# Kernel optimization log

Hardware: AMD Instinct MI355X
Metric: run time of the kernel (lower is better)

The kernel has to match this reference:

```python
import math
import jax, jax.numpy as jnp
import numpy as np

B, S, H = 4, 2048, 1024      # batch, seq_len, hidden_size
E, K, I = 8, 2, 1024         # n_routed_experts, top_k, expert intermediate
NSH = 2                      # n_shared_experts -> shared intermediate = NSH*I
CF, RSF = 1.25, 1.0          # capacity_factor, routed_scaling_factor


def setup_inputs() -> dict:
    key = jax.random.key(0)
    ks = jax.random.split(key, 8)
    w = lambda k, sh: jax.random.normal(k, sh, dtype=jnp.float32) * 0.02
    return {
        "hidden_states": jax.random.normal(ks[0], (B, S, H), dtype=jnp.float32),
        "gate_w":  w(ks[1], (E, H)),          # router weight (torch Linear layout)
        "we_gate": w(ks[2], (E, I, H)),       # per-expert gate_proj
        "we_up":   w(ks[3], (E, I, H)),       # per-expert up_proj
        "we_down": w(ks[4], (E, H, I)),       # per-expert down_proj
        "ws_gate": w(ks[5], (NSH * I, H)),    # shared expert gate_proj
        "ws_up":   w(ks[6], (NSH * I, H)),
        "ws_down": w(ks[7], (H, NSH * I)),
    }


def reference(hidden_states, gate_w, we_gate, we_up, we_down, ws_gate, ws_up, ws_down):
    orig_shape = hidden_states.shape
    x = hidden_states.reshape(-1, H)                       # [N, H]
    N = x.shape[0]

    # ---- gate (fp32 softmax + top-k, normalized, scaled) ----
    logits = x.astype(jnp.float32) @ gate_w.astype(jnp.float32).T   # [N, E]
    scores = jax.nn.softmax(logits, axis=-1)
    topk_w, topk_idx = jax.lax.top_k(scores, K)                      # [N, K]
    topk_w = topk_w / (topk_w.sum(-1, keepdims=True) + 1e-20) * RSF  # norm_topk_prob

    # ---- capacity masking: position of each (token,k) slot within its expert ----
    capacity = math.ceil(CF * N * K / E)
    flat = topk_idx.reshape(-1)                                      # [N*K]
    one_hot = jax.nn.one_hot(flat, E, dtype=jnp.int32)               # [N*K, E]
    pos = jnp.cumsum(one_hot, axis=0) - 1                            # running count per expert
    pos_tok = jnp.take_along_axis(pos, flat[:, None], axis=1)[:, 0]  # [N*K]
    keep = (pos_tok < capacity).reshape(N, K)
    topk_w = topk_w * keep.astype(topk_w.dtype)

    # ---- combine weights per (token, expert); dropped slots contribute 0 ----
    comb = jnp.zeros((N, E), jnp.float32).at[jnp.arange(N)[:, None], topk_idx].add(topk_w)

    # ---- routed experts: dense SwiGLU per expert, weighted combine ----
    g = jnp.einsum('nh,eih->nei', x, we_gate)                        # [N, E, I]
    u = jnp.einsum('nh,eih->nei', x, we_up)
    eo = jnp.einsum('nei,ehi->neh', jax.nn.silu(g) * u, we_down)     # [N, E, H]
    y = jnp.einsum('neh,ne->nh', eo, comb)                           # [N, H]

    # ---- shared experts ----
    sh = (jax.nn.silu(x @ ws_gate.T) * (x @ ws_up.T)) @ ws_down.T    # [N, H]

    return (y + sh).reshape(orig_shape)
```

## Files before the change

### kernel.cpp

```cpp
#include <hip/hip_runtime.h>

typedef unsigned short u16;

#define NTOK 8192
#define HD   1024
#define NEXP 8
#define CAP  2560

typedef __bf16 bf16x8 __attribute__((ext_vector_type(8)));
typedef float  f32x4  __attribute__((ext_vector_type(4)));

__device__ __forceinline__ u16 f2bf(float f){
  union { float f; unsigned u; } v; v.f = f;
  return (u16)((v.u + 0x7fffu + ((v.u >> 16) & 1u)) >> 16);
}
__device__ __forceinline__ float bf2f(u16 h){
  union { unsigned u; float f; } v; v.u = ((unsigned)h) << 16; return v.f;
}

__device__ __forceinline__ void async16(const void* g, void* l){
  __builtin_amdgcn_global_load_lds((__attribute__((address_space(1))) void*)(g),
                                   (__attribute__((address_space(3))) void*)(l), 16, 0, 0);
}

__global__ __launch_bounds__(256)
void prep_kernel(const float* __restrict__ x, const float* __restrict__ gate_w,
                 const float* __restrict__ we_gate, const float* __restrict__ we_up,
                 const float* __restrict__ we_down, const float* __restrict__ ws_gate,
                 const float* __restrict__ ws_up, const float* __restrict__ ws_down,
                 u16* __restrict__ x_bf, u16* __restrict__ wg_bf, u16* __restrict__ wu_bf,
                 u16* __restrict__ wd_bf, u16* __restrict__ wsg_bf, u16* __restrict__ wsu_bf,
                 u16* __restrict__ wsd_bf,
                 int* __restrict__ topk_idx, float* __restrict__ topk_w){
  __shared__ float gw[NEXP * HD];
  int bid = blockIdx.x;
  int t = threadIdx.x;
  if (bid < 2048){
    for (int i = t; i < NEXP * HD; i += 256) gw[i] = gate_w[i];
    __syncthreads();
    int wave = t >> 6, l = t & 63;
    int tok = bid * 4 + wave;
    const float* xr = x + (size_t)tok * HD;
    double acc[NEXP];
#pragma unroll
    for (int e = 0; e < NEXP; e++) acc[e] = 0.0;
    for (int j = 0; j < 16; j++){
      int h = j * 64 + l;
      double xv = (double)xr[h];
#pragma unroll
      for (int e = 0; e < NEXP; e++) acc[e] += xv * (double)gw[e * HD + h];
    }
#pragma unroll
    for (int e = 0; e < NEXP; e++){
      double v = acc[e];
#pragma unroll
      for (int off = 32; off > 0; off >>= 1) v += __shfl_down(v, off, 64);
      acc[e] = v;
    }
    if (l == 0){
      int i0 = 0; double l0 = acc[0];
#pragma unroll
      for (int e = 1; e < NEXP; e++) if (acc[e] > l0){ l0 = acc[e]; i0 = e; }
      int i1 = -1; double l1 = -1e300;
#pragma unroll
      for (int e = 0; e < NEXP; e++) if (e != i0 && acc[e] > l1){ l1 = acc[e]; i1 = e; }
      double e1 = exp(l1 - l0);
      double s  = 1.0 + e1;
      topk_idx[tok * 2 + 0] = i0;
      topk_idx[tok * 2 + 1] = i1;
      topk_w [tok * 2 + 0] = (float)(1.0 / s);
      topk_w [tok * 2 + 1] = (float)(e1 / s);
    }
  } else {
    long long g = (long long)(bid - 2048) * 256 + t;
    const float4* s; ushort4* d; long long off;
    if      (g <  2097152){ s = (const float4*)x;       d = (ushort4*)x_bf;   off = 0; }
    else if (g <  4194304){ s = (const float4*)we_gate; d = (ushort4*)wg_bf;  off = 2097152; }
    else if (g <  6291456){ s = (const float4*)we_up;   d = (ushort4*)wu_bf;  off = 4194304; }
    else if (g <  8388608){ s = (const float4*)we_down; d = (ushort4*)wd_bf;  off = 6291456; }
    else if (g <  8912896){ s = (const float4*)ws_gate; d = (ushort4*)wsg_bf; off = 8388608; }
    else if (g <  9437184){ s = (const float4*)ws_up;   d = (ushort4*)wsu_bf; off = 8912896; }
    else                  { s = (const float4*)ws_down; d = (ushort4*)wsd_bf; off = 9437184; }
    long long i = g - off;
    float4 v = s[i];
    ushort4 o;
    o.x = f2bf(v.x); o.y = f2bf(v.y); o.z = f2bf(v.z); o.w = f2bf(v.w);
    d[i] = o;
  }
}

__global__ __launch_bounds__(256)
void scan_p1(const int* __restrict__ topk_idx, int* __restrict__ chunk_hist){
  __shared__ int wcnt[4 * NEXP];
  int t = threadIdx.x, w = t >> 6, l = t & 63;
  int my_e = topk_idx[blockIdx.x * 256 + t];
#pragma unroll
  for (int e = 0; e < NEXP; e++){
    unsigned long long m = __ballot(my_e == e);
    if (l == e) wcnt[w * NEXP + e] = __popcll(m);
  }
  __syncthreads();
  if (t < NEXP){
    int s = 0;
#pragma unroll
    for (int w2 = 0; w2 < 4; w2++) s += wcnt[w2 * NEXP + t];
    chunk_hist[blockIdx.x * NEXP + t] = s;
  }
}

__global__ __launch_bounds__(256)
void scan_p2(const int* __restrict__ topk_idx, const float* __restrict__ topk_w,
             const int* __restrict__ chunk_hist,
             int* __restrict__ tok_list, float* __restrict__ w_list,
             int* __restrict__ slot_map, int* __restrict__ ne){
  __shared__ int hist_s[64 * NEXP];
  __shared__ int base_s[NEXP];
  __shared__ int wcnt[4 * NEXP];
  int t = threadIdx.x, w = t >> 6, l = t & 63;
  int chunk = blockIdx.x;
#pragma unroll
  for (int i = 0; i < 2; i++) hist_s[i * 256 + t] = chunk_hist[i * 256 + t];
  __syncthreads();
  if (t < NEXP){
    int b = 0, tot = 0;
    for (int c = 0; c < 64; c++){
      if (c == chunk) b = tot;
      tot += hist_s[c * NEXP + t];
    }
    base_s[t] = b;
    if (chunk == 0) ne[t] = tot < CAP ? tot : CAP;
  }
  int slot = chunk * 256 + t;
  int my_e = topk_idx[slot];
  float my_w = topk_w[slot];
  unsigned long long mymask = 0;
#pragma unroll
  for (int e = 0; e < NEXP; e++){
    unsigned long long m = __ballot(my_e == e);
    if (my_e == e) mymask = m;
    if (l == e) wcnt[w * NEXP + e] = __popcll(m);
  }
  __syncthreads();
  if (t < NEXP){
    int run = 0;
#pragma unroll
    for (int w2 = 0; w2 < 4; w2++){ int v = wcnt[w2 * NEXP + t]; wcnt[w2 * NEXP + t] = run; run += v; }
  }
  __syncthreads();
  int pos = base_s[my_e] + wcnt[w * NEXP + my_e] + __popcll(mymask & ((1ull << l) - 1ull));
  if (pos < CAP){
    tok_list[my_e * CAP + pos] = slot >> 1;
    w_list [my_e * CAP + pos] = my_w;
    slot_map[slot] = my_e * CAP + pos;
  } else {
    slot_map[slot] = -1;
  }
}

__global__ __launch_bounds__(256)
void gu_kernel(const u16* __restrict__ x_bf,
               const u16* __restrict__ wg, const u16* __restrict__ wu,
               const u16* __restrict__ wsg, const u16* __restrict__ wsu,
               u16* __restrict__ Hr, u16* __restrict__ Hs,
               const int* __restrict__ tok_list, const int* __restrict__ ne)
{
  __shared__ u16 As[128 * 64];
  __shared__ u16 Bs[128 * 64];

  const int bid = blockIdx.x;
  const bool routed = bid < 2560;
  int m0, n0, ldc, n_valid;
  const u16 *B0, *B1;
  u16* C;
  const int* tl = nullptr;
  if (routed){
    int e = bid & 7, r = bid >> 3;
    m0 = (r >> 4) * 128; n0 = (r & 15) * 64;
    B0 = wg + (size_t)e * (1024 * 1024);
    B1 = wu + (size_t)e * (1024 * 1024);
    C  = Hr + (size_t)e * (CAP * 1024);
    ldc = 1024;
    n_valid = ne[e];
    tl = tok_list + e * CAP;
    if (m0 >= n_valid) return;
  } else {
    int b2 = bid - 2560;
    n0 = (b2 / 64) * 64; m0 = (b2 % 64) * 128;
    B0 = wsg; B1 = wsu; C = Hs; ldc = 2048; n_valid = 1 << 30;
  }

  const int tid = threadIdx.x;
  const int wv  = tid >> 6;
  const int l   = tid & 63;
  const int lr  = l >> 3;
  const int cb  = (l & 7) ^ lr;

  const u16* aptr[4];
  const u16* bptr[4];
#pragma unroll
  for (int i = 0; i < 4; i++){
    int chunk = i * 4 + wv;
    int arow  = m0 + chunk * 8 + lr;
    if (routed){
      int r2 = arow < n_valid ? arow : (n_valid - 1);
      aptr[i] = x_bf + (size_t)tl[r2] * 1024 + cb * 8;
    } else {
      aptr[i] = x_bf + (size_t)arow * 1024 + cb * 8;
    }
    int rn = chunk * 8 + lr;
    int w  = rn >> 6;
    int jq = (rn >> 4) & 3;
    int rl = rn & 15;
    int icol = n0 + w * 32 + (jq & 1) * 16 + rl;
    bptr[i] = ((jq < 2) ? B0 : B1) + (size_t)icol * 1024 + cb * 8;
  }

  const int wm = wv & 1, wn = wv >> 1;
  const int col = l & 15, quad = l >> 4;
  const int rr = col & 7, ch = col >> 3;

  f32x4 acc[4][4];
#pragma unroll
  for (int i = 0; i < 4; i++)
#pragma unroll
    for (int j = 0; j < 4; j++)
      acc[i][j] = (f32x4){0.f, 0.f, 0.f, 0.f};

  for (int k0 = 0; k0 < 1024; k0 += 64){
#pragma unroll
    for (int i = 0; i < 4; i++){
      int chunk = i * 4 + wv;
      async16(aptr[i] + k0, &As[chunk * 512 + l * 8]);
      async16(bptr[i] + k0, &Bs[chunk * 512 + l * 8]);
    }
    __syncthreads();
#pragma unroll
    for (int s = 0; s < 2; s++){
      const int so = (rr * 8 + ((quad + s * 4) ^ rr)) * 8;
      bf16x8 a[4], b[4];
#pragma unroll
      for (int i = 0; i < 4; i++) a[i] = *(const bf16x8*)&As[(wm * 8 + i * 2 + ch) * 512 + so];
#pragma unroll
      for (int j = 0; j < 4; j++) b[j] = *(const bf16x8*)&Bs[(wn * 8 + j * 2 + ch) * 512 + so];
#pragma unroll
      for (int i = 0; i < 4; i++)
#pragma unroll
        for (int j = 0; j < 4; j++)
          acc[i][j] = __builtin_amdgcn_mfma_f32_16x16x32_bf16(a[i], b[j], acc[i][j], 0, 0, 0);
    }
    __syncthreads();
  }

#pragma unroll
  for (int i = 0; i < 4; i++)
#pragma unroll
    for (int r = 0; r < 4; r++){
      int row = m0 + wm * 64 + i * 16 + quad * 4 + r;
#pragma unroll
      for (int j = 0; j < 2; j++){
        int cg = n0 + wn * 32 + j * 16 + col;
        float g = acc[i][j][r], u = acc[i][j + 2][r];
        float h = (g / (1.f + __expf(-g))) * u;
        C[(size_t)row * ldc + cg] = f2bf(h);
      }
    }
}

__global__ __launch_bounds__(256)
void down_kernel(const u16* __restrict__ Hr, const u16* __restrict__ wd,
                 const u16* __restrict__ Hs, const u16* __restrict__ wsd,
                 u16* __restrict__ Ebuf, float* __restrict__ out,
                 const float* __restrict__ w_list, const int* __restrict__ ne)
{
  __shared__ u16 As[128 * 64];
  __shared__ u16 Bs[128 * 64];

  const int bid = blockIdx.x;
  const bool routed = bid < 1280;
  int m0, n0, n_valid, K, e = 0;
  const u16 *Ab, *Bb;
  if (routed){
    e = bid & 7; int r = bid >> 3;
    m0 = (r >> 3) * 128; n0 = (r & 7) * 128;
    Ab = Hr + (size_t)e * (CAP * 1024);
    Bb = wd + (size_t)e * (1024 * 1024);
    K = 1024;
    n_valid = ne[e];
    if (m0 >= n_valid) return;
  } else {
    int b2 = bid - 1280;
    n0 = (b2 & 7) * 128; m0 = (b2 >> 3) * 128;
    Ab = Hs; Bb = wsd; K = 2048; n_valid = 1 << 30;
  }

  const int tid = threadIdx.x;
  const int wv  = tid >> 6;
  const int l   = tid & 63;
  const int lr  = l >> 3;
  const int cb  = (l & 7) ^ lr;

  const u16* aptr[4];
  const u16* bptr[4];
#pragma unroll
  for (int i = 0; i < 4; i++){
    int chunk = i * 4 + wv;
    aptr[i] = Ab + (size_t)(m0 + chunk * 8 + lr) * K + cb * 8;
    bptr[i] = Bb + (size_t)(n0 + chunk * 8 + lr) * K + cb * 8;
  }

  const int wm = wv & 1, wn = wv >> 1;
  const int col = l & 15, quad = l >> 4;
  const int rr = col & 7, ch = col >> 3;

  f32x4 acc[4][4];
#pragma unroll
  for (int i = 0; i < 4; i++)
#pragma unroll
    for (int j = 0; j < 4; j++)
      acc[i][j] = (f32x4){0.f, 0.f, 0.f, 0.f};

  for (int k0 = 0; k0 < K; k0 += 64){
#pragma unroll
    for (int i = 0; i < 4; i++){
      int chunk = i * 4 + wv;
      async16(aptr[i] + k0, &As[chunk * 512 + l * 8]);
      async16(bptr[i] + k0, &Bs[chunk * 512 + l * 8]);
    }
    __syncthreads();
#pragma unroll
    for (int s = 0; s < 2; s++){
      const int so = (rr * 8 + ((quad + s * 4) ^ rr)) * 8;
      bf16x8 a[4], b[4];
#pragma unroll
      for (int i = 0; i < 4; i++) a[i] = *(const bf16x8*)&As[(wm * 8 + i * 2 + ch) * 512 + so];
#pragma unroll
      for (int j = 0; j < 4; j++) b[j] = *(const bf16x8*)&Bs[(wn * 8 + j * 2 + ch) * 512 + so];
#pragma unroll
      for (int i = 0; i < 4; i++)
#pragma unroll
        for (int j = 0; j < 4; j++)
          acc[i][j] = __builtin_amdgcn_mfma_f32_16x16x32_bf16(a[i], b[j], acc[i][j], 0, 0, 0);
    }
    __syncthreads();
  }

  if (routed){
    u16* C = Ebuf + (size_t)e * (CAP * 1024);
    const float* wl = w_list + e * CAP;
#pragma unroll
    for (int i = 0; i < 4; i++)
#pragma unroll
      for (int r = 0; r < 4; r++){
        int row = m0 + wm * 64 + i * 16 + quad * 4 + r;
        if (row < n_valid){
          float wgt = wl[row];
#pragma unroll
          for (int j = 0; j < 4; j++){
            int cg = n0 + wn * 64 + j * 16 + col;
            C[(size_t)row * 1024 + cg] = f2bf(wgt * acc[i][j][r]);
          }
        }
      }
  } else {
#pragma unroll
    for (int i = 0; i < 4; i++)
#pragma unroll
      for (int r = 0; r < 4; r++){
        int row = m0 + wm * 64 + i * 16 + quad * 4 + r;
#pragma unroll
        for (int j = 0; j < 4; j++){
          int cg = n0 + wn * 64 + j * 16 + col;
          out[(size_t)row * 1024 + cg] = acc[i][j][r];
        }
      }
  }
}

__global__ __launch_bounds__(256)
void combine_kernel(float* __restrict__ out, const u16* __restrict__ Ebuf,
                    const int* __restrict__ slot_map){
  long long g = (long long)blockIdx.x * 256 + threadIdx.x;
  int row = (int)(g >> 8);
  int c4  = (int)(g & 255);
  int s0 = slot_map[row * 2 + 0];
  int s1 = slot_map[row * 2 + 1];
  float4 v = ((float4*)out)[g];
  if (s0 >= 0){
    ushort4 a = ((const ushort4*)Ebuf)[(size_t)s0 * 256 + c4];
    v.x += bf2f(a.x); v.y += bf2f(a.y); v.z += bf2f(a.z); v.w += bf2f(a.w);
  }
  if (s1 >= 0){
    ushort4 a = ((const ushort4*)Ebuf)[(size_t)s1 * 256 + c4];
    v.x += bf2f(a.x); v.y += bf2f(a.y); v.z += bf2f(a.z); v.w += bf2f(a.w);
  }
  ((float4*)out)[g] = v;
}

extern "C" void kernel_launch(void* const* d_in, const int* in_sizes, int n_in,
                              void* d_out, int out_size, void* d_ws, size_t ws_size,
                              hipStream_t stream){
  const float* x       = (const float*)d_in[0];
  const float* gate_w  = (const float*)d_in[1];
  const float* we_gate = (const float*)d_in[2];
  const float* we_up   = (const float*)d_in[3];
  const float* we_down = (const float*)d_in[4];
  const float* ws_gate = (const float*)d_in[5];
  const float* ws_up   = (const float*)d_in[6];
  const float* ws_down = (const float*)d_in[7];
  float* out = (float*)d_out;

  char* p = (char*)d_ws;
  u16* x_bf   = (u16*)p; p += (size_t)NTOK * HD * 2;
  u16* wg_bf  = (u16*)p; p += (size_t)NEXP * 1024 * 1024 * 2;
  u16* wu_bf  = (u16*)p; p += (size_t)NEXP * 1024 * 1024 * 2;
  u16* wsg_bf = (u16*)p; p += (size_t)2048 * 1024 * 2;
  u16* wsu_bf = (u16*)p; p += (size_t)2048 * 1024 * 2;
  u16* wd_bf  = (u16*)p; p += (size_t)NEXP * 1024 * 1024 * 2;
  u16* wsd_bf = (u16*)p; p += (size_t)1024 * 2048 * 2;
  u16* Hr     = (u16*)p; p += (size_t)NEXP * CAP * 1024 * 2;
  u16* Hs     = (u16*)p; p += (size_t)NTOK * 2048 * 2;
  int*   topk_idx   = (int*)p;   p += (size_t)NTOK * 2 * 4;
  float* topk_w     = (float*)p; p += (size_t)NTOK * 2 * 4;
  int*   tok_list   = (int*)p;   p += (size_t)NEXP * CAP * 4;
  float* w_list     = (float*)p; p += (size_t)NEXP * CAP * 4;
  int*   slot_map   = (int*)p;   p += (size_t)NTOK * 2 * 4;
  int*   chunk_hist = (int*)p;   p += 64 * NEXP * 4;
  int*   ne         = (int*)p;   p += 128;
  u16* Ebuf = wg_bf;

  prep_kernel<<<dim3(40960), dim3(256), 0, stream>>>(
      x, gate_w, we_gate, we_up, we_down, ws_gate, ws_up, ws_down,
      x_bf, wg_bf, wu_bf, wd_bf, wsg_bf, wsu_bf, wsd_bf, topk_idx, topk_w);

  scan_p1<<<dim3(64), dim3(256), 0, stream>>>(topk_idx, chunk_hist);
  scan_p2<<<dim3(64), dim3(256), 0, stream>>>(topk_idx, topk_w, chunk_hist,
                                              tok_list, w_list, slot_map, ne);

  gu_kernel<<<dim3(4608), dim3(256), 0, stream>>>(
      x_bf, wg_bf, wu_bf, wsg_bf, wsu_bf, Hr, Hs, tok_list, ne);

  down_kernel<<<dim3(1792), dim3(256), 0, stream>>>(
      Hr, wd_bf, Hs, wsd_bf, Ebuf, out, w_list, ne);

  combine_kernel<<<dim3(8192), dim3(256), 0, stream>>>(out, Ebuf, slot_map);
}
```

Measured before the change: 486.5 us.

## Overlap down-proj weight conversion with gate/up GEMM and merge scan kernels

Moves the fp32-to-bf16 conversion of the routed and shared down-projection weights out of the prep kernel and into extra trailing blocks of the gate/up GEMM kernel, so that memory-bound conversion can run alongside GEMM tiles. It also fuses the two-pass routing scan into one kernel, where each block recomputes the full per-chunk histogram itself. This removes a launch and shortens the serial prep phase, at the cost of redundant histogram work in every scan block and conversion blocks that compete with GEMM blocks for memory bandwidth.

```diff
diff --git a/kernel.cpp b/kernel.cpp
--- a/kernel.cpp
+++ b/kernel.cpp
@@ -26,11 +26,9 @@
 __global__ __launch_bounds__(256)
 void prep_kernel(const float* __restrict__ x, const float* __restrict__ gate_w,
                  const float* __restrict__ we_gate, const float* __restrict__ we_up,
-                 const float* __restrict__ we_down, const float* __restrict__ ws_gate,
-                 const float* __restrict__ ws_up, const float* __restrict__ ws_down,
+                 const float* __restrict__ ws_gate, const float* __restrict__ ws_up,
                  u16* __restrict__ x_bf, u16* __restrict__ wg_bf, u16* __restrict__ wu_bf,
-                 u16* __restrict__ wd_bf, u16* __restrict__ wsg_bf, u16* __restrict__ wsu_bf,
-                 u16* __restrict__ wsd_bf,
+                 u16* __restrict__ wsg_bf, u16* __restrict__ wsu_bf,
                  int* __restrict__ topk_idx, float* __restrict__ topk_w){
   __shared__ float gw[NEXP * HD];
   int bid = blockIdx.x;
@@ -77,10 +75,8 @@
     if      (g <  2097152){ s = (const float4*)x;       d = (ushort4*)x_bf;   off = 0; }
     else if (g <  4194304){ s = (const float4*)we_gate; d = (ushort4*)wg_bf;  off = 2097152; }
     else if (g <  6291456){ s = (const float4*)we_up;   d = (ushort4*)wu_bf;  off = 4194304; }
-    else if (g <  8388608){ s = (const float4*)we_down; d = (ushort4*)wd_bf;  off = 6291456; }
-    else if (g <  8912896){ s = (const float4*)ws_gate; d = (ushort4*)wsg_bf; off = 8388608; }
-    else if (g <  9437184){ s = (const float4*)ws_up;   d = (ushort4*)wsu_bf; off = 8912896; }
-    else                  { s = (const float4*)ws_down; d = (ushort4*)wsd_bf; off = 9437184; }
+    else if (g <  6815744){ s = (const float4*)ws_gate; d = (ushort4*)wsg_bf; off = 6291456; }
+    else                  { s = (const float4*)ws_up;   d = (ushort4*)wsu_bf; off = 6815744; }
     long long i = g - off;
     float4 v = s[i];
     ushort4 o;
@@ -90,36 +86,27 @@
 }
 
 __global__ __launch_bounds__(256)
-void scan_p1(const int* __restrict__ topk_idx, int* __restrict__ chunk_hist){
-  __shared__ int wcnt[4 * NEXP];
-  int t = threadIdx.x, w = t >> 6, l = t & 63;
-  int my_e = topk_idx[blockIdx.x * 256 + t];
-#pragma unroll
-  for (int e = 0; e < NEXP; e++){
-    unsigned long long m = __ballot(my_e == e);
-    if (l == e) wcnt[w * NEXP + e] = __popcll(m);
-  }
-  __syncthreads();
-  if (t < NEXP){
-    int s = 0;
-#pragma unroll
-    for (int w2 = 0; w2 < 4; w2++) s += wcnt[w2 * NEXP + t];
-    chunk_hist[blockIdx.x * NEXP + t] = s;
-  }
-}
-
-__global__ __launch_bounds__(256)
-void scan_p2(const int* __restrict__ topk_idx, const float* __restrict__ topk_w,
-             const int* __restrict__ chunk_hist,
-             int* __restrict__ tok_list, float* __restrict__ w_list,
-             int* __restrict__ slot_map, int* __restrict__ ne){
+void scan_kernel(const int* __restrict__ topk_idx, const float* __restrict__ topk_w,
+                 int* __restrict__ tok_list, float* __restrict__ w_list,
+                 int* __restrict__ slot_map, int* __restrict__ ne){
   __shared__ int hist_s[64 * NEXP];
   __shared__ int base_s[NEXP];
   __shared__ int wcnt[4 * NEXP];
   int t = threadIdx.x, w = t >> 6, l = t & 63;
   int chunk = blockIdx.x;
-#pragma unroll
-  for (int i = 0; i < 2; i++) hist_s[i * 256 + t] = chunk_hist[i * 256 + t];
+  for (int cc = w * 16; cc < w * 16 + 16; cc++){
+    int cnt = 0;
+#pragma unroll
+    for (int g = 0; g < 4; g++){
+      int eg = topk_idx[cc * 256 + g * 64 + l];
+#pragma unroll
+      for (int e = 0; e < NEXP; e++){
+        unsigned long long m = __ballot(eg == e);
+        if (l == e) cnt += __popcll(m);
+      }
+    }
+    if (l < NEXP) hist_s[cc * NEXP + l] = cnt;
+  }
   __syncthreads();
   if (t < NEXP){
     int b = 0, tot = 0;
@@ -162,12 +149,29 @@
                const u16* __restrict__ wg, const u16* __restrict__ wu,
                const u16* __restrict__ wsg, const u16* __restrict__ wsu,
                u16* __restrict__ Hr, u16* __restrict__ Hs,
-               const int* __restrict__ tok_list, const int* __restrict__ ne)
+               const int* __restrict__ tok_list, const int* __restrict__ ne,
+               const float* __restrict__ we_down, const float* __restrict__ ws_down,
+               u16* __restrict__ wd_bf, u16* __restrict__ wsd_bf)
 {
   __shared__ u16 As[128 * 64];
   __shared__ u16 Bs[128 * 64];
 
   const int bid = blockIdx.x;
+  const int tid = threadIdx.x;
+
+  if (bid >= 4608){
+    long long g = (long long)(bid - 4608) * 256 + tid;
+    const float4* s; ushort4* d; long long off;
+    if (g < 2097152){ s = (const float4*)we_down; d = (ushort4*)wd_bf;  off = 0; }
+    else            { s = (const float4*)ws_down; d = (ushort4*)wsd_bf; off = 2097152; }
+    long long i = g - off;
+    float4 v = s[i];
+    ushort4 o;
+    o.x = f2bf(v.x); o.y = f2bf(v.y); o.z = f2bf(v.z); o.w = f2bf(v.w);
+    d[i] = o;
+    return;
+  }
+
   const bool routed = bid < 2560;
   int m0, n0, ldc, n_valid;
   const u16 *B0, *B1;
@@ -189,7 +193,6 @@
     B0 = wsg; B1 = wsu; C = Hs; ldc = 2048; n_valid = 1 << 30;
   }
 
-  const int tid = threadIdx.x;
   const int wv  = tid >> 6;
   const int l   = tid & 63;
   const int lr  = l >> 3;
@@ -424,20 +427,19 @@
   int*   tok_list   = (int*)p;   p += (size_t)NEXP * CAP * 4;
   float* w_list     = (float*)p; p += (size_t)NEXP * CAP * 4;
   int*   slot_map   = (int*)p;   p += (size_t)NTOK * 2 * 4;
-  int*   chunk_hist = (int*)p;   p += 64 * NEXP * 4;
   int*   ne         = (int*)p;   p += 128;
   u16* Ebuf = wg_bf;
 
-  prep_kernel<<<dim3(40960), dim3(256), 0, stream>>>(
-      x, gate_w, we_gate, we_up, we_down, ws_gate, ws_up, ws_down,
-      x_bf, wg_bf, wu_bf, wd_bf, wsg_bf, wsu_bf, wsd_bf, topk_idx, topk_w);
-
-  scan_p1<<<dim3(64), dim3(256), 0, stream>>>(topk_idx, chunk_hist);
-  scan_p2<<<dim3(64), dim3(256), 0, stream>>>(topk_idx, topk_w, chunk_hist,
-                                              tok_list, w_list, slot_map, ne);
-
-  gu_kernel<<<dim3(4608), dim3(256), 0, stream>>>(
-      x_bf, wg_bf, wu_bf, wsg_bf, wsu_bf, Hr, Hs, tok_list, ne);
+  prep_kernel<<<dim3(30720), dim3(256), 0, stream>>>(
+      x, gate_w, we_gate, we_up, ws_gate, ws_up,
+      x_bf, wg_bf, wu_bf, wsg_bf, wsu_bf, topk_idx, topk_w);
+
+  scan_kernel<<<dim3(64), dim3(256), 0, stream>>>(topk_idx, topk_w,
+                                                  tok_list, w_list, slot_map, ne);
+
+  gu_kernel<<<dim3(14848), dim3(256), 0, stream>>>(
+      x_bf, wg_bf, wu_bf, wsg_bf, wsu_bf, Hr, Hs, tok_list, ne,
+      we_down, ws_down, wd_bf, wsd_bf);
 
   down_kernel<<<dim3(1792), dim3(256), 0, stream>>>(
       Hr, wd_bf, Hs, wsd_bf, Ebuf, out, w_list, ne);
```

New measurement: 487.6 us. About the same (+0.2%).
